# Performance work log

Hardware: AMD Instinct MI355X
Metric: run time of the kernel (lower is better)

## Reference

```python
import jax, jax.numpy as jnp
import numpy as np

N_EMBD = 2048
N_HEAD = 16
N_HIDDEN = 5632  # find_multiple(int(2*4*2048/3), 256)
EPS = 1e-5
BETA = 1.0


def rmsnorm(x, scale):
    # mean of squares computed in fp32 as in the torch code
    norm = jnp.mean(x.astype(jnp.float32) ** 2, axis=-1, keepdims=True)
    x_normed = x * jax.lax.rsqrt(norm + EPS)
    return (scale * x_normed).astype(x.dtype)


def setup_inputs() -> dict:
    key = jax.random.key(0)
    ks = jax.random.split(key, 9)
    B, T, C = 1, 2048, N_EMBD
    s = lambda k, shape, fan: jax.random.normal(k, shape, jnp.float32) * (1.0 / np.sqrt(fan))
    return {
        "x": jax.random.normal(ks[0], (B, T, C), jnp.float32),
        "alibi": jax.random.normal(ks[1], (N_HEAD, T, T), jnp.float32),
        "w_attn": s(ks[2], (C, 3 * C), C),   # c_attn weight (in, out) layout
        "w_proj": s(ks[3], (C, C), C),
        "w_fc1": s(ks[4], (C, N_HIDDEN), C),
        "w_fc2": s(ks[5], (C, N_HIDDEN), C),
        "w_mlp_proj": s(ks[6], (N_HIDDEN, C), N_HIDDEN),
        "rms1_scale": jnp.ones((C,), jnp.float32),
        "rms2_scale": jnp.ones((C,), jnp.float32),
    }


def attention(x, alibi, w_attn, w_proj):
    B, T, C = x.shape
    hd = C // N_HEAD
    qkv = x @ w_attn  # [B,T,3C]
    q, k, v = jnp.split(qkv, 3, axis=-1)
    q = q.reshape(B, T, N_HEAD, hd).transpose(0, 2, 1, 3)  # [B,H,T,hd]
    k = k.reshape(B, T, N_HEAD, hd).transpose(0, 2, 1, 3)
    v = v.reshape(B, T, N_HEAD, hd).transpose(0, 2, 1, 3)
    scale = 1.0 / np.sqrt(hd)
    scores = jnp.einsum("bhqd,bhkd->bhqk", q, k) * scale + BETA * alibi  # [B,H,T,T]
    causal = jnp.tril(jnp.ones((T, T), bool))
    scores = jnp.where(causal, scores, -jnp.inf)
    attn = jax.nn.softmax(scores, axis=-1)
    y = jnp.einsum("bhqk,bhkd->bhqd", attn, v)
    y = y.transpose(0, 2, 1, 3).reshape(B, T, C)
    return y @ w_proj


def mlp(x, w_fc1, w_fc2, w_mlp_proj):
    return (jax.nn.silu(x @ w_fc1) * (x @ w_fc2)) @ w_mlp_proj


def reference(x, alibi, w_attn, w_proj, w_fc1, w_fc2, w_mlp_proj, rms1_scale, rms2_scale):
    x = x + attention(rmsnorm(x, rms1_scale), alibi, w_attn, w_proj)
    x = x + mlp(rmsnorm(x, rms2_scale), w_fc1, w_fc2, w_mlp_proj)
    return x
```

## Files before the change

kernel.cpp:

```cpp
#include <hip/hip_runtime.h>
#include <stdint.h>

typedef __attribute__((ext_vector_type(4))) float f32x4;
typedef __attribute__((ext_vector_type(8))) __bf16 bf8_t;
typedef __attribute__((ext_vector_type(8))) uint16_t u16x8;

typedef __attribute__((address_space(1))) uint8_t as1_u8;
typedef __attribute__((address_space(3))) uint8_t as3_u8;

__device__ inline void async_copy16(const void* g, void* l) {
  __builtin_amdgcn_global_load_lds((const as1_u8*)g, (as3_u8*)l, 16, 0, 0);
}

__device__ inline uint16_t f2bf(float f) {
  uint32_t u = __builtin_bit_cast(uint32_t, f);
  u = (u + 0x7fff + ((u >> 16) & 1)) >> 16;
  return (uint16_t)u;
}
__device__ inline float bf2f(uint16_t h) {
  uint32_t u = ((uint32_t)h) << 16;
  return __builtin_bit_cast(float, u);
}
__device__ inline int swz(int r) { return (((r & 7) ^ ((r >> 3) & 7)) << 4); }
__device__ inline int vswz(int r) { return ((r & 7) << 4); }

__global__ __launch_bounds__(256) void rmsnorm_kernel(const float* __restrict__ X,
                                                      const float* __restrict__ S,
                                                      uint16_t* __restrict__ O) {
  const int row = blockIdx.x;
  const int tid = threadIdx.x;
  const float* xr = X + (size_t)row * 2048;
  float4 v1 = ((const float4*)xr)[tid * 2];
  float4 v2 = ((const float4*)xr)[tid * 2 + 1];
  float ss = v1.x * v1.x + v1.y * v1.y + v1.z * v1.z + v1.w * v1.w +
             v2.x * v2.x + v2.y * v2.y + v2.z * v2.z + v2.w * v2.w;
  #pragma unroll
  for (int m = 1; m < 64; m <<= 1) ss += __shfl_xor(ss, m);
  __shared__ float wsum[4];
  if ((tid & 63) == 0) wsum[tid >> 6] = ss;
  __syncthreads();
  float tot = wsum[0] + wsum[1] + wsum[2] + wsum[3];
  float inv = rsqrtf(tot * (1.0f / 2048.0f) + 1e-5f);
  const int base = tid * 8;
  const float* sc = S + base;
  float xs[8] = {v1.x, v1.y, v1.z, v1.w, v2.x, v2.y, v2.z, v2.w};
  u16x8 o;
  #pragma unroll
  for (int j = 0; j < 8; j++) o[j] = f2bf(xs[j] * inv * sc[j]);
  *(u16x8*)(O + (size_t)row * 2048 + base) = o;
}

__device__ inline void transpose_tile(const float* __restrict__ W, uint16_t* __restrict__ WT,
                                      int K, int N, int bx, int by, int tid) {
  __shared__ float tile[64][65];
  const int n0 = bx * 64, k0 = by * 64;
  const int lr = tid >> 4;
  const int lc = (tid & 15) * 4;
  #pragma unroll
  for (int i = 0; i < 4; i++) {
    const float4 v = *(const float4*)&W[(size_t)(k0 + lr + i * 16) * N + n0 + lc];
    tile[lr + i * 16][lc] = v.x;
    tile[lr + i * 16][lc + 1] = v.y;
    tile[lr + i * 16][lc + 2] = v.z;
    tile[lr + i * 16][lc + 3] = v.w;
  }
  __syncthreads();
  const int tn = tid >> 3;
  const int tk = (tid & 7) * 8;
  #pragma unroll
  for (int i = 0; i < 2; i++) {
    u16x8 o;
    #pragma unroll
    for (int j = 0; j < 8; j++) o[j] = f2bf(tile[tk + j][tn + i * 32]);
    *(u16x8*)&WT[(size_t)(n0 + tn + i * 32) * K + k0 + tk] = o;
  }
}

__global__ __launch_bounds__(256) void transpose_all(
    const float* __restrict__ w_attn, const float* __restrict__ w_proj,
    const float* __restrict__ w_fc1, const float* __restrict__ w_fc2,
    const float* __restrict__ w_mp,
    uint16_t* __restrict__ wt_attn, uint16_t* __restrict__ wt_proj,
    uint16_t* __restrict__ wt_fc1, uint16_t* __restrict__ wt_fc2,
    uint16_t* __restrict__ wt_mp) {
  int idx = blockIdx.x;
  const int tid = threadIdx.x;
  if (idx < 3072) {
    transpose_tile(w_attn, wt_attn, 2048, 6144, idx % 96, idx / 96, tid);
  } else if (idx < 4096) {
    idx -= 3072;
    transpose_tile(w_proj, wt_proj, 2048, 2048, idx % 32, idx / 32, tid);
  } else if (idx < 6912) {
    idx -= 4096;
    transpose_tile(w_fc1, wt_fc1, 2048, 5632, idx % 88, idx / 88, tid);
  } else if (idx < 9728) {
    idx -= 6912;
    transpose_tile(w_fc2, wt_fc2, 2048, 5632, idx % 88, idx / 88, tid);
  } else {
    idx -= 9728;
    transpose_tile(w_mp, wt_mp, 5632, 2048, idx % 32, idx / 32, tid);
  }
}

__global__ __launch_bounds__(256) void transpose_v(const uint16_t* __restrict__ qkv,
                                                   uint16_t* __restrict__ vT) {
  __shared__ uint16_t tile[64][68];
  const int t0 = blockIdx.x * 64;
  const int c0 = blockIdx.y * 64;
  const int tid = threadIdx.x;
  const int lr = tid >> 3;
  const int lc = (tid & 7) * 8;
  #pragma unroll
  for (int i = 0; i < 2; i++) {
    const int r = lr + i * 32;
    u16x8 v = *(const u16x8*)&qkv[(size_t)(t0 + r) * 6144 + 4096 + c0 + lc];
    #pragma unroll
    for (int j = 0; j < 8; j++) tile[lc + j][r] = v[j];
  }
  __syncthreads();
  #pragma unroll
  for (int i = 0; i < 2; i++) {
    const int c = lr + i * 32;
    u16x8 o = *(const u16x8*)&tile[c][lc];
    *(u16x8*)&vT[(size_t)(c0 + c) * 2048 + t0 + lc] = o;
  }
}

enum { EPI_BF16 = 0, EPI_ADDF32 = 1, EPI_SILUMUL = 2 };

__device__ inline void gemm_epi(int EPI, void* Cout, const void* RES, size_t idx, float v) {
  if (EPI == EPI_BF16) {
    ((uint16_t*)Cout)[idx] = f2bf(v);
  } else if (EPI == EPI_ADDF32) {
    ((float*)Cout)[idx] = ((const float*)RES)[idx] + v;
  } else {
    const float g = bf2f(((const uint16_t*)RES)[idx]);
    const float sg = g / (1.0f + __expf(-g));
    ((uint16_t*)Cout)[idx] = f2bf(sg * v);
  }
}

template <int EPI>
__global__ __launch_bounds__(256, 2) void gemm_bt(const uint16_t* __restrict__ A,
                                                  const uint16_t* __restrict__ BT,
                                                  void* __restrict__ Cout,
                                                  const void* __restrict__ RES,
                                                  int M, int N, int K) {
  __shared__ uint16_t As[128 * 64];
  __shared__ uint16_t Bs[128 * 64];
  const int tid = threadIdx.x;
  const int lane = tid & 63;
  const int w = tid >> 6;
  const int l15 = lane & 15, l4 = lane >> 4;
  const int m0 = blockIdx.y * 128, n0 = blockIdx.x * 128;
  const int wr = w >> 1, wc = w & 1;

  f32x4 acc[4][4];
  #pragma unroll
  for (int i = 0; i < 4; i++)
    #pragma unroll
    for (int j = 0; j < 4; j++) acc[i][j] = 0.0f;

  for (int kk = 0; kk < K; kk += 64) {
    __syncthreads();
    #pragma unroll
    for (int s = 0; s < 4; s++) {
      const int bu = s * 256 + w * 64;
      const int u = bu + lane;
      const int row = u >> 3;
      const int ch = (u & 7) ^ (row & 7);
      async_copy16(A + (size_t)(m0 + row) * K + kk + ch * 8, (char*)As + bu * 16);
      async_copy16(BT + (size_t)(n0 + row) * K + kk + ch * 8, (char*)Bs + bu * 16);
    }
    __syncthreads();
    bf8_t a[4][2], b[4][2];
    #pragma unroll
    for (int mi = 0; mi < 4; mi++)
      #pragma unroll
      for (int ks = 0; ks < 2; ks++) {
        const int R = wr * 64 + mi * 16 + l15;
        a[mi][ks] = *(const bf8_t*)((const char*)As + R * 128 + (((ks * 4 + l4) ^ (R & 7)) * 16));
      }
    #pragma unroll
    for (int ni = 0; ni < 4; ni++)
      #pragma unroll
      for (int ks = 0; ks < 2; ks++) {
        const int R = wc * 64 + ni * 16 + l15;
        b[ni][ks] = *(const bf8_t*)((const char*)Bs + R * 128 + (((ks * 4 + l4) ^ (R & 7)) * 16));
      }
    #pragma unroll
    for (int mi = 0; mi < 4; mi++)
      #pragma unroll
      for (int ni = 0; ni < 4; ni++)
        #pragma unroll
        for (int ks = 0; ks < 2; ks++)
          acc[mi][ni] = __builtin_amdgcn_mfma_f32_16x16x32_bf16(a[mi][ks], b[ni][ks],
                                                                acc[mi][ni], 0, 0, 0);
  }

  #pragma unroll
  for (int mi = 0; mi < 4; mi++) {
    #pragma unroll
    for (int ni = 0; ni < 4; ni++) {
      #pragma unroll
      for (int r = 0; r < 4; r++) {
        const int row = m0 + wr * 64 + mi * 16 + l4 * 4 + r;
        const int col = n0 + wc * 64 + ni * 16 + l15;
        gemm_epi(EPI, Cout, RES, (size_t)row * N + col, acc[mi][ni][r]);
      }
    }
  }
}

template <int EPI>
__global__ __launch_bounds__(256, 3) void gemm_bt64(const uint16_t* __restrict__ A,
                                                    const uint16_t* __restrict__ BT,
                                                    void* __restrict__ Cout,
                                                    const void* __restrict__ RES,
                                                    int M, int N, int K) {
  __shared__ uint16_t As[128 * 64];
  __shared__ uint16_t Bs[64 * 64];
  const int tid = threadIdx.x;
  const int lane = tid & 63;
  const int w = tid >> 6;
  const int l15 = lane & 15, l4 = lane >> 4;
  const int m0 = blockIdx.y * 128, n0 = blockIdx.x * 64;

  f32x4 acc[2][4];
  #pragma unroll
  for (int i = 0; i < 2; i++)
    #pragma unroll
    for (int j = 0; j < 4; j++) acc[i][j] = 0.0f;

  for (int kk = 0; kk < K; kk += 64) {
    __syncthreads();
    #pragma unroll
    for (int s = 0; s < 4; s++) {
      const int bu = s * 256 + w * 64;
      const int u = bu + lane;
      const int row = u >> 3;
      const int ch = (u & 7) ^ (row & 7);
      async_copy16(A + (size_t)(m0 + row) * K + kk + ch * 8, (char*)As + bu * 16);
    }
    #pragma unroll
    for (int s = 0; s < 2; s++) {
      const int bu = s * 256 + w * 64;
      const int u = bu + lane;
      const int row = u >> 3;
      const int ch = (u & 7) ^ (row & 7);
      async_copy16(BT + (size_t)(n0 + row) * K + kk + ch * 8, (char*)Bs + bu * 16);
    }
    __syncthreads();
    bf8_t a[2][2], b[4][2];
    #pragma unroll
    for (int mi = 0; mi < 2; mi++)
      #pragma unroll
      for (int ks = 0; ks < 2; ks++) {
        const int R = w * 32 + mi * 16 + l15;
        a[mi][ks] = *(const bf8_t*)((const char*)As + R * 128 + (((ks * 4 + l4) ^ (R & 7)) * 16));
      }
    #pragma unroll
    for (int ni = 0; ni < 4; ni++)
      #pragma unroll
      for (int ks = 0; ks < 2; ks++) {
        const int R = ni * 16 + l15;
        b[ni][ks] = *(const bf8_t*)((const char*)Bs + R * 128 + (((ks * 4 + l4) ^ (R & 7)) * 16));
      }
    #pragma unroll
    for (int mi = 0; mi < 2; mi++)
      #pragma unroll
      for (int ni = 0; ni < 4; ni++)
        #pragma unroll
        for (int ks = 0; ks < 2; ks++)
          acc[mi][ni] = __builtin_amdgcn_mfma_f32_16x16x32_bf16(a[mi][ks], b[ni][ks],
                                                                acc[mi][ni], 0, 0, 0);
  }

  #pragma unroll
  for (int mi = 0; mi < 2; mi++) {
    #pragma unroll
    for (int ni = 0; ni < 4; ni++) {
      #pragma unroll
      for (int r = 0; r < 4; r++) {
        const int row = m0 + w * 32 + mi * 16 + l4 * 4 + r;
        const int col = n0 + ni * 16 + l15;
        gemm_epi(EPI, Cout, RES, (size_t)row * N + col, acc[mi][ni][r]);
      }
    }
  }
}

#define PART_STRIDE (64 * 128 + 128)
__global__ __launch_bounds__(256, 2) void attn_part(const uint16_t* __restrict__ qkv,
                                                    const uint16_t* __restrict__ vT,
                                                    const float* __restrict__ alibi,
                                                    float* __restrict__ part) {
  const int p = blockIdx.x;
  const int qt = 31 - blockIdx.y;
  const int h = blockIdx.z;
  const int c = (qt + 4) >> 2;
  const int start = p * c;
  const int end = min((p + 1) * c, qt + 1);
  if (start >= end) return;

  const int tid = threadIdx.x;
  const int lane = tid & 63;
  const int w = tid >> 6;
  const int l15 = lane & 15, l4 = lane >> 4;

  __shared__ uint16_t Ks[2][64 * 128];
  __shared__ uint16_t Vs[2][128 * 64];
  __shared__ uint16_t Ps[4][16 * 64];

  const float scale = 0.08838834764831845f;

  auto stage = [&](int kv0, int b) {
    #pragma unroll
    for (int i = 0; i < 4; i++) {
      const int u = tid + i * 256;
      const int r = u >> 4;
      const int cc = (u & 15) ^ ((r & 7) ^ ((r >> 3) & 7));
      async_copy16(qkv + (size_t)(kv0 + r) * 6144 + 2048 + h * 128 + cc * 8,
                   (char*)Ks[b] + u * 16);
    }
    #pragma unroll
    for (int i = 0; i < 4; i++) {
      const int u = tid + i * 256;
      const int r = u >> 3;
      const int cc = (u & 7) ^ (r & 7);
      async_copy16(vT + (size_t)(h * 128 + r) * 2048 + kv0 + cc * 8,
                   (char*)Vs[b] + u * 16);
    }
  };
  auto load_al = [&](int kv0, float (&al)[4][4]) {
    #pragma unroll
    for (int r = 0; r < 4; r++) {
      const size_t rowb = ((size_t)h * 2048 + (qt * 64 + w * 16 + l4 * 4 + r)) * 2048;
      #pragma unroll
      for (int nf = 0; nf < 4; nf++)
        al[nf][r] = alibi[rowb + kv0 + nf * 16 + l15];
    }
  };

  const int qrow = qt * 64 + w * 16 + l15;
  bf8_t qf[4];
  #pragma unroll
  for (int kc = 0; kc < 4; kc++)
    qf[kc] = *(const bf8_t*)(qkv + (size_t)qrow * 6144 + h * 128 + kc * 32 + l4 * 8);

  f32x4 accy[8];
  #pragma unroll
  for (int i = 0; i < 8; i++) accy[i] = 0.0f;
  float mrun[4], lrun[4];
  #pragma unroll
  for (int r = 0; r < 4; r++) { mrun[r] = -1e30f; lrun[r] = 0.0f; }

  stage(start * 64, 0);
  float al[4][4];
  load_al(start * 64, al);

  for (int kvt = start; kvt < end; kvt++) {
    const int b = (kvt - start) & 1;
    const int kv0 = kvt * 64;
    __syncthreads();

    const int kvn = (kvt + 1 < end) ? (kvt + 1) : kvt;
    float aln[4][4];
    load_al(kvn * 64, aln);
    stage(kvn * 64, b ^ 1);

    float s[4][4];
    #pragma unroll
    for (int nf = 0; nf < 4; nf++) {
      f32x4 sa = 0.0f;
      const int krow = nf * 16 + l15;
      __builtin_amdgcn_s_setprio(1);
      #pragma unroll
      for (int kc = 0; kc < 4; kc++) {
        bf8_t kb = *(const bf8_t*)((const char*)Ks[b] +
                                   ((krow * 256 + kc * 64 + l4 * 16) ^ swz(krow)));
        sa = __builtin_amdgcn_mfma_f32_16x16x32_bf16(qf[kc], kb, sa, 0, 0, 0);
      }
      __builtin_amdgcn_s_setprio(0);
      const int kvcol = kv0 + nf * 16 + l15;
      #pragma unroll
      for (int r = 0; r < 4; r++) {
        const int q = qt * 64 + w * 16 + l4 * 4 + r;
        float sv = sa[r] * scale + al[nf][r];
        if (kvcol > q) sv = -1e30f;
        s[nf][r] = sv;
      }
    }

    #pragma unroll
    for (int r = 0; r < 4; r++) {
      float rm = fmaxf(fmaxf(s[0][r], s[1][r]), fmaxf(s[2][r], s[3][r]));
      rm = fmaxf(rm, __shfl_xor(rm, 1));
      rm = fmaxf(rm, __shfl_xor(rm, 2));
      rm = fmaxf(rm, __shfl_xor(rm, 4));
      rm = fmaxf(rm, __shfl_xor(rm, 8));
      const float mnew = fmaxf(mrun[r], rm);
      const float alpha = __expf(mrun[r] - mnew);
      mrun[r] = mnew;
      float rs = 0.0f;
      #pragma unroll
      for (int nf = 0; nf < 4; nf++) {
        const float pp = __expf(s[nf][r] - mnew);
        s[nf][r] = pp;
        rs += pp;
      }
      rs += __shfl_xor(rs, 1);
      rs += __shfl_xor(rs, 2);
      rs += __shfl_xor(rs, 4);
      rs += __shfl_xor(rs, 8);
      lrun[r] = lrun[r] * alpha + rs;
      #pragma unroll
      for (int df = 0; df < 8; df++) accy[df][r] *= alpha;
    }

    #pragma unroll
    for (int nf = 0; nf < 4; nf++) {
      #pragma unroll
      for (int r = 0; r < 4; r++) {
        const int rq = l4 * 4 + r;
        const int bo = (rq * 128 + (nf * 16 + l15) * 2) ^ vswz(rq);
        *(uint16_t*)((char*)Ps[w] + bo) = f2bf(s[nf][r]);
      }
    }

    __builtin_amdgcn_s_setprio(1);
    #pragma unroll
    for (int kk = 0; kk < 2; kk++) {
      bf8_t pa = *(const bf8_t*)((const char*)Ps[w] +
                                 ((l15 * 128 + kk * 64 + l4 * 16) ^ vswz(l15)));
      #pragma unroll
      for (int df = 0; df < 8; df++) {
        const int vr = df * 16 + l15;
        bf8_t vb = *(const bf8_t*)((const char*)Vs[b] +
                                   ((vr * 128 + kk * 64 + l4 * 16) ^ vswz(vr)));
        accy[df] = __builtin_amdgcn_mfma_f32_16x16x32_bf16(pa, vb, accy[df], 0, 0, 0);
      }
    }
    __builtin_amdgcn_s_setprio(0);

    #pragma unroll
    for (int nf = 0; nf < 4; nf++)
      #pragma unroll
      for (int r = 0; r < 4; r++) al[nf][r] = aln[nf][r];
  }

  float* pb = part + (size_t)(((h * 32 + qt) * 4) + p) * PART_STRIDE;
  #pragma unroll
  for (int df = 0; df < 8; df++) {
    #pragma unroll
    for (int r = 0; r < 4; r++) {
      const int row = w * 16 + l4 * 4 + r;
      pb[row * 128 + df * 16 + l15] = accy[df][r];
    }
  }
  if (l15 == 0) {
    #pragma unroll
    for (int r = 0; r < 4; r++) {
      const int row = w * 16 + l4 * 4 + r;
      pb[8192 + row] = mrun[r];
      pb[8192 + 64 + row] = lrun[r];
    }
  }
}

__global__ __launch_bounds__(256) void attn_merge(const float* __restrict__ part,
                                                  uint16_t* __restrict__ Y) {
  const int qt = blockIdx.x;
  const int h = blockIdx.y;
  const int c = (qt + 4) >> 2;
  const int cnt = (qt + c) / c;
  const int tid = threadIdx.x;
  const int row = tid >> 2;
  const int cg = (tid & 3) * 32;

  const float* pb = part + (size_t)((h * 32 + qt) * 4) * PART_STRIDE;

  float m_p[4], w_p[4];
  float M = -1e30f;
  for (int p = 0; p < cnt; p++) {
    m_p[p] = pb[p * PART_STRIDE + 8192 + row];
    M = fmaxf(M, m_p[p]);
  }
  float L = 0.0f;
  for (int p = 0; p < cnt; p++) {
    w_p[p] = __expf(m_p[p] - M);
    L += w_p[p] * pb[p * PART_STRIDE + 8192 + 64 + row];
  }
  const float invL = 1.0f / L;

  uint16_t* yr = Y + (size_t)(qt * 64 + row) * 2048 + h * 128 + cg;
  #pragma unroll
  for (int j = 0; j < 32; j += 8) {
    f32x4 s0 = 0.0f, s1 = 0.0f;
    for (int p = 0; p < cnt; p++) {
      const float* ap = pb + p * PART_STRIDE + row * 128 + cg + j;
      s0 += w_p[p] * *(const f32x4*)ap;
      s1 += w_p[p] * *(const f32x4*)(ap + 4);
    }
    u16x8 o;
    #pragma unroll
    for (int e = 0; e < 4; e++) { o[e] = f2bf(s0[e] * invL); o[e + 4] = f2bf(s1[e] * invL); }
    *(u16x8*)(yr + j) = o;
  }
}

extern "C" void kernel_launch(void* const* d_in, const int* in_sizes, int n_in,
                              void* d_out, int out_size, void* d_ws, size_t ws_size,
                              hipStream_t stream) {
  const float* x      = (const float*)d_in[0];
  const float* alibi  = (const float*)d_in[1];
  const float* w_attn = (const float*)d_in[2];
  const float* w_proj = (const float*)d_in[3];
  const float* w_fc1  = (const float*)d_in[4];
  const float* w_fc2  = (const float*)d_in[5];
  const float* w_mp   = (const float*)d_in[6];
  const float* rms1   = (const float*)d_in[7];
  const float* rms2   = (const float*)d_in[8];
  float* out = (float*)d_out;

  char* ws = (char*)d_ws;
  uint16_t* xn      = (uint16_t*)(ws + 0);
  uint16_t* qkv     = (uint16_t*)(ws + 8388608);
  uint16_t* y       = (uint16_t*)(ws + 33554432);
  uint16_t* g1      = (uint16_t*)(ws + 41943040);
  uint16_t* hbuf    = (uint16_t*)(ws + 65011712);
  uint16_t* wt_attn = (uint16_t*)(ws + 88080384);
  uint16_t* wt_proj = (uint16_t*)(ws + 113246208);
  uint16_t* wt_fc1  = (uint16_t*)(ws + 121634816);
  uint16_t* wt_fc2  = (uint16_t*)(ws + 144703488);
  uint16_t* wt_mp   = (uint16_t*)(ws + 167772160);
  uint16_t* vT      = (uint16_t*)(ws + 190840832);
  float*    part    = (float*)(ws + 199229440);

  transpose_all<<<12544, 256, 0, stream>>>(w_attn, w_proj, w_fc1, w_fc2, w_mp,
                                           wt_attn, wt_proj, wt_fc1, wt_fc2, wt_mp);

  rmsnorm_kernel<<<2048, 256, 0, stream>>>(x, rms1, xn);

  gemm_bt<EPI_BF16><<<dim3(6144 / 128, 2048 / 128), 256, 0, stream>>>(
      xn, wt_attn, qkv, nullptr, 2048, 6144, 2048);

  transpose_v<<<dim3(32, 32), 256, 0, stream>>>(qkv, vT);

  attn_part<<<dim3(4, 32, 16), 256, 0, stream>>>(qkv, vT, alibi, part);

  attn_merge<<<dim3(32, 16), 256, 0, stream>>>(part, y);

  gemm_bt64<EPI_ADDF32><<<dim3(2048 / 64, 2048 / 128), 256, 0, stream>>>(
      y, wt_proj, out, x, 2048, 2048, 2048);

  rmsnorm_kernel<<<2048, 256, 0, stream>>>(out, rms2, xn);

  gemm_bt<EPI_BF16><<<dim3(5632 / 128, 2048 / 128), 256, 0, stream>>>(
      xn, wt_fc1, g1, nullptr, 2048, 5632, 2048);

  gemm_bt<EPI_SILUMUL><<<dim3(5632 / 128, 2048 / 128), 256, 0, stream>>>(
      xn, wt_fc2, hbuf, g1, 2048, 5632, 2048);

  gemm_bt64<EPI_ADDF32><<<dim3(2048 / 64, 2048 / 128), 256, 0, stream>>>(
      hbuf, wt_mp, out, out, 2048, 2048, 5632);
}
```

Measured before the change: 491.3 us.

## Fuse fc1 and fc2 GEMMs via interleaved concatenated weights with SiLU-mul epilogue

The fc1 and fc2 weights are transposed into a single concatenated matrix whose rows alternate in 16-row groups, so one GEMM computes both projections. Each tile then holds matching gate and value columns, and the SiLU-times-multiply is applied in registers. This removes the separate fc1 launch, the bf16 g1 intermediate write, and its re-read in the second GEMM. The catch is strided 2-byte scalar stores in the epilogue and a kernel that loads only one stage per iteration without double buffering.

Result: faster. 477.5 us (-2.8%).

```diff
diff --git a/kernel.cpp b/kernel.cpp
--- a/kernel.cpp
+++ b/kernel.cpp
@@ -50,8 +50,8 @@
   *(u16x8*)(O + (size_t)row * 2048 + base) = o;
 }
 
-__device__ inline void transpose_tile(const float* __restrict__ W, uint16_t* __restrict__ WT,
-                                      int K, int N, int bx, int by, int tid) {
+__device__ inline void transpose_tile2(const float* __restrict__ W, uint16_t* __restrict__ WT,
+                                       int K, int N, int bx, int by, int tid, int catoff) {
   __shared__ float tile[64][65];
   const int n0 = bx * 64, k0 = by * 64;
   const int lr = tid >> 4;
@@ -72,7 +72,9 @@
     u16x8 o;
     #pragma unroll
     for (int j = 0; j < 8; j++) o[j] = f2bf(tile[tk + j][tn + i * 32]);
-    *(u16x8*)&WT[(size_t)(n0 + tn + i * 32) * K + k0 + tk] = o;
+    const int n = n0 + tn + i * 32;
+    const int row = (catoff < 0) ? n : (((n >> 4) << 5) + catoff + (n & 15));
+    *(u16x8*)&WT[(size_t)row * K + k0 + tk] = o;
   }
 }
 
@@ -81,24 +83,23 @@
     const float* __restrict__ w_fc1, const float* __restrict__ w_fc2,
     const float* __restrict__ w_mp,
     uint16_t* __restrict__ wt_attn, uint16_t* __restrict__ wt_proj,
-    uint16_t* __restrict__ wt_fc1, uint16_t* __restrict__ wt_fc2,
-    uint16_t* __restrict__ wt_mp) {
+    uint16_t* __restrict__ wt_cat, uint16_t* __restrict__ wt_mp) {
   int idx = blockIdx.x;
   const int tid = threadIdx.x;
   if (idx < 3072) {
-    transpose_tile(w_attn, wt_attn, 2048, 6144, idx % 96, idx / 96, tid);
+    transpose_tile2(w_attn, wt_attn, 2048, 6144, idx % 96, idx / 96, tid, -1);
   } else if (idx < 4096) {
     idx -= 3072;
-    transpose_tile(w_proj, wt_proj, 2048, 2048, idx % 32, idx / 32, tid);
+    transpose_tile2(w_proj, wt_proj, 2048, 2048, idx % 32, idx / 32, tid, -1);
   } else if (idx < 6912) {
     idx -= 4096;
-    transpose_tile(w_fc1, wt_fc1, 2048, 5632, idx % 88, idx / 88, tid);
+    transpose_tile2(w_fc1, wt_cat, 2048, 5632, idx % 88, idx / 88, tid, 0);
   } else if (idx < 9728) {
     idx -= 6912;
-    transpose_tile(w_fc2, wt_fc2, 2048, 5632, idx % 88, idx / 88, tid);
+    transpose_tile2(w_fc2, wt_cat, 2048, 5632, idx % 88, idx / 88, tid, 16);
   } else {
     idx -= 9728;
-    transpose_tile(w_mp, wt_mp, 5632, 2048, idx % 32, idx / 32, tid);
+    transpose_tile2(w_mp, wt_mp, 5632, 2048, idx % 32, idx / 32, tid, -1);
   }
 }
 
@@ -207,6 +208,79 @@
         const int row = m0 + wr * 64 + mi * 16 + l4 * 4 + r;
         const int col = n0 + wc * 64 + ni * 16 + l15;
         gemm_epi(EPI, Cout, RES, (size_t)row * N + col, acc[mi][ni][r]);
+      }
+    }
+  }
+}
+
+__global__ __launch_bounds__(256, 2) void gemm_cat(const uint16_t* __restrict__ A,
+                                                   const uint16_t* __restrict__ BT,
+                                                   uint16_t* __restrict__ Cout,
+                                                   int M, int K) {
+  __shared__ uint16_t As[128 * 64];
+  __shared__ uint16_t Bs[128 * 64];
+  const int tid = threadIdx.x;
+  const int lane = tid & 63;
+  const int w = tid >> 6;
+  const int l15 = lane & 15, l4 = lane >> 4;
+  const int m0 = blockIdx.y * 128, n0 = blockIdx.x * 128;
+  const int wr = w >> 1, wc = w & 1;
+
+  f32x4 acc[4][4];
+  #pragma unroll
+  for (int i = 0; i < 4; i++)
+    #pragma unroll
+    for (int j = 0; j < 4; j++) acc[i][j] = 0.0f;
+
+  for (int kk = 0; kk < K; kk += 64) {
+    __syncthreads();
+    #pragma unroll
+    for (int s = 0; s < 4; s++) {
+      const int bu = s * 256 + w * 64;
+      const int u = bu + lane;
+      const int row = u >> 3;
+      const int ch = (u & 7) ^ (row & 7);
+      async_copy16(A + (size_t)(m0 + row) * K + kk + ch * 8, (char*)As + bu * 16);
+      async_copy16(BT + (size_t)(n0 + row) * K + kk + ch * 8, (char*)Bs + bu * 16);
+    }
+    __syncthreads();
+    bf8_t a[4][2], b[4][2];
+    #pragma unroll
+    for (int mi = 0; mi < 4; mi++)
+      #pragma unroll
+      for (int ks = 0; ks < 2; ks++) {
+        const int R = wr * 64 + mi * 16 + l15;
+        a[mi][ks] = *(const bf8_t*)((const char*)As + R * 128 + (((ks * 4 + l4) ^ (R & 7)) * 16));
+      }
+    #pragma unroll
+    for (int ni = 0; ni < 4; ni++)
+      #pragma unroll
+      for (int ks = 0; ks < 2; ks++) {
+        const int R = wc * 64 + ni * 16 + l15;
+        b[ni][ks] = *(const bf8_t*)((const char*)Bs + R * 128 + (((ks * 4 + l4) ^ (R & 7)) * 16));
+      }
+    #pragma unroll
+    for (int mi = 0; mi < 4; mi++)
+      #pragma unroll
+      for (int ni = 0; ni < 4; ni++)
+        #pragma unroll
+        for (int ks = 0; ks < 2; ks++)
+          acc[mi][ni] = __builtin_amdgcn_mfma_f32_16x16x32_bf16(a[mi][ks], b[ni][ks],
+                                                                acc[mi][ni], 0, 0, 0);
+  }
+
+  #pragma unroll
+  for (int mi = 0; mi < 4; mi++) {
+    #pragma unroll
+    for (int p = 0; p < 2; p++) {
+      const int col = n0 / 2 + ((wc * 4 + 2 * p) >> 1) * 16 + l15;
+      #pragma unroll
+      for (int r = 0; r < 4; r++) {
+        const int row = m0 + wr * 64 + mi * 16 + l4 * 4 + r;
+        const float g = acc[mi][2 * p][r];
+        const float h = acc[mi][2 * p + 1][r];
+        const float sg = g / (1.0f + __expf(-g));
+        Cout[(size_t)row * 5632 + col] = f2bf(sg * h);
       }
     }
   }
@@ -527,18 +601,16 @@
   uint16_t* xn      = (uint16_t*)(ws + 0);
   uint16_t* qkv     = (uint16_t*)(ws + 8388608);
   uint16_t* y       = (uint16_t*)(ws + 33554432);
-  uint16_t* g1      = (uint16_t*)(ws + 41943040);
   uint16_t* hbuf    = (uint16_t*)(ws + 65011712);
   uint16_t* wt_attn = (uint16_t*)(ws + 88080384);
   uint16_t* wt_proj = (uint16_t*)(ws + 113246208);
-  uint16_t* wt_fc1  = (uint16_t*)(ws + 121634816);
-  uint16_t* wt_fc2  = (uint16_t*)(ws + 144703488);
+  uint16_t* wt_cat  = (uint16_t*)(ws + 121634816);
   uint16_t* wt_mp   = (uint16_t*)(ws + 167772160);
   uint16_t* vT      = (uint16_t*)(ws + 190840832);
   float*    part    = (float*)(ws + 199229440);
 
   transpose_all<<<12544, 256, 0, stream>>>(w_attn, w_proj, w_fc1, w_fc2, w_mp,
-                                           wt_attn, wt_proj, wt_fc1, wt_fc2, wt_mp);
+                                           wt_attn, wt_proj, wt_cat, wt_mp);
 
   rmsnorm_kernel<<<2048, 256, 0, stream>>>(x, rms1, xn);
 
@@ -556,11 +628,8 @@
 
   rmsnorm_kernel<<<2048, 256, 0, stream>>>(out, rms2, xn);
 
-  gemm_bt<EPI_BF16><<<dim3(5632 / 128, 2048 / 128), 256, 0, stream>>>(
-      xn, wt_fc1, g1, nullptr, 2048, 5632, 2048);
-
-  gemm_bt<EPI_SILUMUL><<<dim3(5632 / 128, 2048 / 128), 256, 0, stream>>>(
-      xn, wt_fc2, hbuf, g1, 2048, 5632, 2048);
+  gemm_cat<<<dim3(11264 / 128, 2048 / 128), 256, 0, stream>>>(
+      xn, wt_cat, hbuf, 2048, 2048);
 
   gemm_bt64<EPI_ADDF32><<<dim3(2048 / 64, 2048 / 128), 256, 0, stream>>>(
       hbuf, wt_mp, out, out, 2048, 2048, 5632);
```
